# Kernel tuning notes

Measured on AMD Instinct MI355X. Metric: run time of the kernel, lower is better.

The kernel has to match this reference:

```python
import jax, jax.numpy as jnp
import numpy as np

# Problem dims (production MPPI-style rollout batch)
B, H, L, S, O = 512, 32, 7, 5, 8  # batch, horizon, links, spheres/link, world objs
DIST_THRESHOLD = 0.1


def setup_inputs() -> dict:
    key = jax.random.key(0)
    ks = jax.random.split(key, 6)
    # forward args
    link_pos_seq = jax.random.normal(ks[0], (B, H, L, 3), dtype=jnp.float32) * 0.5
    link_rot_seq = jax.random.normal(ks[1], (B, H, L, 3, 3), dtype=jnp.float32)
    # learned/config params: robot collision spheres (link frame) + world sphere primitives
    sphere_offsets = jax.random.normal(ks[2], (L, S, 3), dtype=jnp.float32) * 0.1
    sphere_radii = jax.random.uniform(ks[3], (L, S), dtype=jnp.float32, minval=0.02, maxval=0.08)
    obj_centers = jax.random.normal(ks[4], (O, 3), dtype=jnp.float32) * 0.6
    obj_radii = jax.random.uniform(ks[5], (O,), dtype=jnp.float32, minval=0.05, maxval=0.3)
    weight = jnp.asarray(1.0, dtype=jnp.float32)
    return {
        "link_pos_seq": link_pos_seq,
        "link_rot_seq": link_rot_seq,
        "sphere_offsets": sphere_offsets,
        "sphere_radii": sphere_radii,
        "obj_centers": obj_centers,
        "obj_radii": obj_radii,
        "weight": weight,
    }


def reference(link_pos_seq, link_rot_seq, sphere_offsets, sphere_radii,
              obj_centers, obj_radii, weight):
    b, h, l, _ = link_pos_seq.shape
    n = b * h
    pos = link_pos_seq.reshape(n, l, 3)          # [N,L,3]
    rot = link_rot_seq.reshape(n, l, 3, 3)       # [N,L,3,3]
    # transform link-frame collision spheres into world frame: c = R @ o + p
    centers = jnp.einsum('nlij,lsj->nlsi', rot, sphere_offsets) + pos[:, :, None, :]  # [N,L,S,3]
    # sphere-vs-world-sphere signed distance (positive = penetration)
    diff = centers[:, :, :, None, :] - obj_centers[None, None, None, :, :]  # [N,L,S,O,3]
    d = jnp.sqrt(jnp.sum(diff * diff, axis=-1))                             # [N,L,S,O]
    signed = (sphere_radii[None, :, :, None] + obj_radii[None, None, None, :]) - d
    dist = jnp.max(signed, axis=(2, 3)).reshape(b, h, l)  # worst sphere/obj per link
    # clamp-scale-sum-weight chain from forward()
    dist = jnp.clip(dist + DIST_THRESHOLD, 0.0, 0.2) / 0.25
    cost = weight * jnp.sum(dist, axis=-1)  # [B,H]
    return cost
```

## Files before the change

### kernel.cpp

```cpp
#include <hip/hip_runtime.h>

#define BB 512
#define HH 32
#define LL 7
#define SS 5
#define OO 8
#define NN (BB * HH)
#define DIST_THRESHOLD 0.1f

__global__ __launch_bounds__(64)
void PrimitiveCollisionCost_19533511262442_kernel(
    const float* __restrict__ pos,
    const float* __restrict__ rot,
    const float* __restrict__ off,
    const float* __restrict__ srad,
    const float* __restrict__ oc,
    const float* __restrict__ orad,
    const float* __restrict__ weight,
    float* __restrict__ out)
{
    const int n = blockIdx.x * blockDim.x + threadIdx.x;
    if (n >= NN) return;

    const float w = weight[0];
    const float* posn = pos + (size_t)n * (LL * 3);
    const float* rotn = rot + (size_t)n * (LL * 9);

    float cost = 0.0f;

    for (int l = 0; l < LL; ++l) {
        const float px = posn[l * 3 + 0];
        const float py = posn[l * 3 + 1];
        const float pz = posn[l * 3 + 2];

        const float r00 = rotn[l * 9 + 0];
        const float r01 = rotn[l * 9 + 1];
        const float r02 = rotn[l * 9 + 2];
        const float r10 = rotn[l * 9 + 3];
        const float r11 = rotn[l * 9 + 4];
        const float r12 = rotn[l * 9 + 5];
        const float r20 = rotn[l * 9 + 6];
        const float r21 = rotn[l * 9 + 7];
        const float r22 = rotn[l * 9 + 8];

        float best = -1e30f;

#pragma unroll
        for (int s = 0; s < SS; ++s) {
            const float ox = off[(l * SS + s) * 3 + 0];
            const float oy = off[(l * SS + s) * 3 + 1];
            const float oz = off[(l * SS + s) * 3 + 2];
            const float rs = srad[l * SS + s];

            const float cx = r00 * ox + r01 * oy + r02 * oz + px;
            const float cy = r10 * ox + r11 * oy + r12 * oz + py;
            const float cz = r20 * ox + r21 * oy + r22 * oz + pz;

#pragma unroll
            for (int o = 0; o < OO; ++o) {
                const float dx = cx - oc[o * 3 + 0];
                const float dy = cy - oc[o * 3 + 1];
                const float dz = cz - oc[o * 3 + 2];
                const float d  = sqrtf(dx * dx + dy * dy + dz * dz);
                const float sg = rs + orad[o] - d;
                best = fmaxf(best, sg);
            }
        }

        const float dist = fminf(fmaxf(best + DIST_THRESHOLD, 0.0f), 0.2f) * 4.0f;
        cost += dist;
    }

    out[n] = w * cost;
}

extern "C" void kernel_launch(void* const* d_in, const int* in_sizes, int n_in,
                              void* d_out, int out_size, void* d_ws, size_t ws_size,
                              hipStream_t stream) {
    const float* pos    = (const float*)d_in[0];
    const float* rot    = (const float*)d_in[1];
    const float* off    = (const float*)d_in[2];
    const float* srad   = (const float*)d_in[3];
    const float* oc     = (const float*)d_in[4];
    const float* orad   = (const float*)d_in[5];
    const float* weight = (const float*)d_in[6];
    float* out = (float*)d_out;

    constexpr int block = 64;
    constexpr int grid  = (NN + block - 1) / block;

    PrimitiveCollisionCost_19533511262442_kernel<<<grid, block, 0, stream>>>(
        pos, rot, off, srad, oc, orad, weight, out);
}
```

Before: 86.47 us.

## Parallelize links across threads with wavefront shuffle reduction

Assigns one thread per (sample, link) pair, using 8 lanes per sample with one idle lane, instead of one thread looping over all 7 links. Per-link costs are summed with xor shuffles inside each group of 8 lanes, and lane 0 writes the result. The grid grows eightfold and blocks grow to 256 threads, which exposes much more parallelism for the 16K-sample problem and makes neighbouring lanes read neighbouring memory. The cost is one idle lane in eight and a short shuffle reduction.

```diff
diff --git a/kernel.cpp b/kernel.cpp
--- a/kernel.cpp
+++ b/kernel.cpp
@@ -8,7 +8,7 @@
 #define NN (BB * HH)
 #define DIST_THRESHOLD 0.1f
 
-__global__ __launch_bounds__(64)
+__global__ __launch_bounds__(256)
 void PrimitiveCollisionCost_19533511262442_kernel(
     const float* __restrict__ pos,
     const float* __restrict__ rot,
@@ -19,29 +19,29 @@
     const float* __restrict__ weight,
     float* __restrict__ out)
 {
-    const int n = blockIdx.x * blockDim.x + threadIdx.x;
-    if (n >= NN) return;
+    const int t = blockIdx.x * blockDim.x + threadIdx.x;
+    const int n = t >> 3;
+    const int l = t & 7;
 
-    const float w = weight[0];
-    const float* posn = pos + (size_t)n * (LL * 3);
-    const float* rotn = rot + (size_t)n * (LL * 9);
+    float dist = 0.0f;
 
-    float cost = 0.0f;
+    if (l < LL) {
+        const float* posn = pos + (size_t)n * (LL * 3) + l * 3;
+        const float* rotn = rot + (size_t)n * (LL * 9) + l * 9;
 
-    for (int l = 0; l < LL; ++l) {
-        const float px = posn[l * 3 + 0];
-        const float py = posn[l * 3 + 1];
-        const float pz = posn[l * 3 + 2];
+        const float px = posn[0];
+        const float py = posn[1];
+        const float pz = posn[2];
 
-        const float r00 = rotn[l * 9 + 0];
-        const float r01 = rotn[l * 9 + 1];
-        const float r02 = rotn[l * 9 + 2];
-        const float r10 = rotn[l * 9 + 3];
-        const float r11 = rotn[l * 9 + 4];
-        const float r12 = rotn[l * 9 + 5];
-        const float r20 = rotn[l * 9 + 6];
-        const float r21 = rotn[l * 9 + 7];
-        const float r22 = rotn[l * 9 + 8];
+        const float r00 = rotn[0];
+        const float r01 = rotn[1];
+        const float r02 = rotn[2];
+        const float r10 = rotn[3];
+        const float r11 = rotn[4];
+        const float r12 = rotn[5];
+        const float r20 = rotn[6];
+        const float r21 = rotn[7];
+        const float r22 = rotn[8];
 
         float best = -1e30f;
 
@@ -67,11 +67,16 @@
             }
         }
 
-        const float dist = fminf(fmaxf(best + DIST_THRESHOLD, 0.0f), 0.2f) * 4.0f;
-        cost += dist;
+        dist = fminf(fmaxf(best + DIST_THRESHOLD, 0.0f), 0.2f) * 4.0f;
     }
 
-    out[n] = w * cost;
+    dist += __shfl_xor(dist, 1, 64);
+    dist += __shfl_xor(dist, 2, 64);
+    dist += __shfl_xor(dist, 4, 64);
+
+    if (l == 0) {
+        out[n] = weight[0] * dist;
+    }
 }
 
 extern "C" void kernel_launch(void* const* d_in, const int* in_sizes, int n_in,
@@ -86,8 +91,8 @@
     const float* weight = (const float*)d_in[6];
     float* out = (float*)d_out;
 
-    constexpr int block = 64;
-    constexpr int grid  = (NN + block - 1) / block;
+    constexpr int block = 256;
+    constexpr int grid  = (NN * 8) / block;
 
     PrimitiveCollisionCost_19533511262442_kernel<<<grid, block, 0, stream>>>(
         pos, rot, off, srad, oc, orad, weight, out);
```

New measurement: 72.40 us. 16.3% less time.
